# Kernel tuning notes

Measured on AMD Instinct MI355X. Metric: run time of the kernel, lower is better.

The kernel has to match this reference:

```python
import jax, jax.numpy as jnp
import numpy as np

T, N, H, K, A = 256, 8, 512, 16, 4
NUM_ACTIONS = 6
P_SUB = 0.1
LOSS_FACTOR = 0.1


def setup_inputs() -> dict:
    key = jax.random.key(0)
    ks = jax.random.split(key, 14)
    inp = {
        "vision": jax.random.normal(ks[0], (T, N, H), dtype=jnp.float32),
        "belief_features": jax.random.normal(ks[1], (T, N, H), dtype=jnp.float32),
        "actions": jax.random.randint(ks[2], (T, N), 0, NUM_ACTIONS + 1),
        # episode-boundary indices per env, kept in [1, T) to match torch slicing semantics
        "env_zeros": jnp.sort(jax.random.randint(ks[3], (N, 4), 1, T), axis=-1),
        "negative_inds": jax.random.randint(ks[4], (T * N,), 0, T * N),
        # params
        "emb": jax.random.normal(ks[5], (NUM_ACTIONS + 1, A), dtype=jnp.float32) * 0.1,
        "W_ih": jax.random.normal(ks[6], (3 * H, A), dtype=jnp.float32) * 0.1,
        "W_hh": jax.random.normal(ks[7], (3 * H, H), dtype=jnp.float32) * 0.02,
        "b_ih": jnp.zeros((3 * H,), jnp.float32),
        "b_hh": jnp.zeros((3 * H,), jnp.float32),
        "W1": jax.random.normal(ks[8], (32, 2 * H), dtype=jnp.float32) * 0.02,
        "b1": jnp.zeros((32,), jnp.float32),
        "W2": jax.random.normal(ks[9], (1, 32), dtype=jnp.float32) * 0.1,
        "b2": jnp.zeros((1,), jnp.float32),
        "t": T,
        "n": N,
    }
    return inp


def reference(vision, belief_features, actions, env_zeros, negative_inds,
              emb, W_ih, W_hh, b_ih, b_hh, W1, b1, W2, b2, t, n):
    k = K
    h = vision.shape[-1]
    dt = vision.dtype

    positives = vision                                     # (t, n, H)
    negatives = vision.reshape(t * n, h)[negative_inds].reshape(t, n, h)

    # action sequences via unfold: act_seq[m, i*n+e] = padded[i+m, e]
    act_emb = emb[actions]                                 # (t, n, A)
    act_pad = jnp.concatenate([act_emb, jnp.zeros((k - 1, n, A), dt)], axis=0)
    idx = jnp.arange(t)[:, None] + jnp.arange(k)[None, :]  # (t, k)
    act_seq = act_pad[idx].transpose(1, 0, 2, 3).reshape(k, t * n, A)

    # GRU (torch gate order: r, z, n), h0 = belief features per (t,n) position
    h0 = belief_features.reshape(t * n, h)

    def gru_step(hs, x):
        gi = x @ W_ih.T + b_ih
        gh = hs @ W_hh.T + b_hh
        i_r, i_z, i_n = jnp.split(gi, 3, axis=-1)
        h_r, h_z, h_n = jnp.split(gh, 3, axis=-1)
        r = jax.nn.sigmoid(i_r + h_r)
        z = jax.nn.sigmoid(i_z + h_z)
        cand = jnp.tanh(i_n + r * h_n)
        h_new = (1.0 - z) * cand + z * hs
        return h_new, h_new

    _, out_all = jax.lax.scan(gru_step, h0, act_seq)       # (k, t*n, H)
    query_all = out_all.reshape(k, t, n, h).transpose(1, 0, 2, 3)  # (t, k, n, H)

    zpad = jnp.zeros((k, n, h), dt)
    pos_exp = jnp.concatenate([positives[1:], zpad], axis=0)[idx]  # (t, k, n, H)
    neg_exp = jnp.concatenate([negatives[1:], zpad], axis=0)[idx]

    def classify(feat):
        h1 = jax.nn.relu(feat @ W1.T + b1)
        return (h1 @ W2.T + b2)[..., 0]                    # (t, k, n)

    pos_logits = classify(jnp.concatenate([pos_exp, query_all], axis=-1))
    neg_logits = classify(jnp.concatenate([neg_exp, query_all], axis=-1))

    # valid mask: valid_full[r, c, e] then take diagonals valid[i, m, e] = valid_full[i+m, m, e]
    r = jnp.arange(t + k)[:, None, None]                   # (t+k, 1, 1)
    c = jnp.arange(k)[None, :, None]                       # (1, k, 1)
    z = env_zeros[None, None, :, :]                        # (1, 1, n, m)
    zero_hit = jnp.any((z >= (r - c + 1)[..., None]) & (z <= (r + 1)[..., None]), axis=-1)
    valid_full = (r >= c) & (r < t - 1) & (~zero_hit)      # (t+k, k, n)
    valid_mask = valid_full[idx, jnp.arange(k)[None, :]]   # (t, k, n)

    weight = jnp.array([5, 4, 3, 3, 2, 2, 2, 2, 1, 1, 1, 1, 1, 1, 1, 1], dtype=dt)

    # BCE-with-logits: target 1 -> softplus(-x); target 0 -> softplus(x)
    pos_loss = jax.nn.softplus(-pos_logits) * weight[None, :, None]
    neg_loss = jax.nn.softplus(neg_logits) * weight[None, :, None]

    k1, k2 = jax.random.split(jax.random.key(42))
    sub_p = jax.random.uniform(k1, pos_loss.shape) < P_SUB
    sub_n = jax.random.uniform(k2, neg_loss.shape) < P_SUB

    def masked_mean(loss, mask):
        m = mask.astype(dt)
        return jnp.sum(loss * m) / jnp.maximum(jnp.sum(m), 1.0)

    sp = masked_mean(pos_loss, valid_mask & sub_p)
    sn = masked_mean(neg_loss, valid_mask & sub_n)
    return (sp + sn) * LOSS_FACTOR
```

## Files before the change

### kernel.cpp

```cpp
#include <hip/hip_runtime.h>
#include <hip/hip_bf16.h>

#define T_DIM 256
#define KK    16

typedef __attribute__((ext_vector_type(8))) short bf16x8;
typedef __attribute__((ext_vector_type(4))) float f32x4;

#define MFMA16(A, B, C) __builtin_amdgcn_mfma_f32_16x16x32_bf16(A, B, C, 0, 0, 0)
#define SLOT 1048576

__device__ __forceinline__ unsigned short f2b(float x) {
  unsigned u = __float_as_uint(x);
  unsigned r = (u + 0x7FFFu + ((u >> 16) & 1u)) >> 16;
  return (unsigned short)r;
}

__device__ __forceinline__ bf16x8 ld_b128_bypass(const unsigned short* p) {
  bf16x8 r;
  asm volatile("global_load_dwordx4 %0, %1, off sc0 sc1" : "=v"(r) : "v"(p) : "memory");
  return r;
}
__device__ __forceinline__ void st_b128_bypass(unsigned short* p, bf16x8 v) {
  asm volatile("global_store_dwordx4 %0, %1, off sc0 sc1" :: "v"(p), "v"(v) : "memory");
}
__device__ __forceinline__ unsigned ld_u32_bypass(const unsigned* p) {
  unsigned r;
  asm volatile("global_load_dword %0, %1, off sc0 sc1\n\ts_waitcnt vmcnt(0)"
               : "=v"(r) : "v"(p) : "memory");
  return r;
}
__device__ __forceinline__ bf16x8 ld_b128(const unsigned short* p) {
  bf16x8 r;
  asm volatile("global_load_dwordx4 %0, %1, off" : "=v"(r) : "v"(p) : "memory");
  return r;
}
#define WAITVM0() asm volatile("s_waitcnt vmcnt(0)" ::: "memory")

__device__ __forceinline__ void tf2x32(unsigned k0, unsigned k1, unsigned x0, unsigned x1,
                                       unsigned &o0, unsigned &o1) {
  unsigned ks2 = k0 ^ k1 ^ 0x1BD11BDAu;
  x0 += k0; x1 += k1;
#define TFR(R) { x0 += x1; x1 = (x1 << R) | (x1 >> (32 - R)); x1 ^= x0; }
  TFR(13) TFR(15) TFR(26) TFR(6)   x0 += k1;  x1 += ks2 + 1u;
  TFR(17) TFR(29) TFR(16) TFR(24)  x0 += ks2; x1 += k0 + 2u;
  TFR(13) TFR(15) TFR(26) TFR(6)   x0 += k0;  x1 += k1 + 3u;
  TFR(17) TFR(29) TFR(16) TFR(24)  x0 += k1;  x1 += ks2 + 4u;
  TFR(13) TFR(15) TFR(26) TFR(6)   x0 += ks2; x1 += k0 + 5u;
#undef TFR
  o0 = x0; o1 = x1;
}

__global__ void prep(const float* __restrict__ W_hh, const float* __restrict__ W1,
                     const float* __restrict__ emb,  const float* __restrict__ W_ih,
                     const float* __restrict__ b_ih, const float* __restrict__ b_hh,
                     const float* __restrict__ vision, const int* __restrict__ env_zeros,
                     const float* __restrict__ belief,
                     unsigned short* __restrict__ wBf, unsigned short* __restrict__ wQf,
                     float* __restrict__ girz, float* __restrict__ gin,
                     float* __restrict__ projP, unsigned char* __restrict__ maskb,
                     unsigned short* __restrict__ hbS, unsigned* __restrict__ cnt) {
  int b = blockIdx.x, tid = threadIdx.x;
  if (b < 768) {
    int idx = b * 256 + tid;
    int row = idx >> 7, k4 = (idx & 127) << 2;
    float4 v = *(const float4*)(W_hh + ((size_t)row << 9) + k4);
    int gam = row >> 9, sl = (row >> 6) & 7, q = (row >> 4) & 3, col0 = row & 15;
    int kt = k4 >> 5, quad = (k4 >> 3) & 3, e = k4 & 7;
    int F = (sl * 12 + gam * 4 + q) * 16 + kt;
    ushort4 o; o.x = f2b(v.x); o.y = f2b(v.y); o.z = f2b(v.z); o.w = f2b(v.w);
    *(ushort4*)(wBf + ((size_t)F << 9) + ((quad * 16 + col0) << 3) + e) = o;
  } else if (b < 784) {
    int idx = (b - 768) * 256 + tid;
    int f = idx >> 7, k4 = (idx & 127) << 2;
    float4 v = *(const float4*)(W1 + (size_t)f * 1024 + 512 + k4);
    int ft = f >> 4, col0 = f & 15;
    int kt = k4 >> 5, quad = (k4 >> 3) & 3, e = k4 & 7;
    int F = ft * 16 + kt;
    ushort4 o; o.x = f2b(v.x); o.y = f2b(v.y); o.z = f2b(v.z); o.w = f2b(v.w);
    *(ushort4*)(wQf + ((size_t)F << 9) + ((quad * 16 + col0) << 3) + e) = o;
  } else if (b < 816) {
    int idx = (b - 784) * 256 + tid;
    int c = idx & 511, ga = idx >> 9;
    int a = ga & 7, gam = ga >> 3;
    float s = b_ih[gam * 512 + c] + b_hh[gam * 512 + c];
    if (a < 7) {
      #pragma unroll
      for (int k = 0; k < 4; ++k) s += emb[a * 4 + k] * W_ih[(gam * 512 + c) * 4 + k];
    }
    girz[idx] = s;
  } else if (b < 832) {
    int idx = (b - 816) * 256 + tid;
    int c = idx & 511, a = idx >> 9;
    float s = b_ih[1024 + c];
    if (a < 7) {
      #pragma unroll
      for (int k = 0; k < 4; ++k) s += emb[a * 4 + k] * W_ih[(1024 + c) * 4 + k];
    }
    gin[idx] = s;
  } else if (b < 1088) {
    int e = (b - 832) * 256 + tid;
    int s = e >> 5, f = e & 31;
    const float4* vr = (const float4*)(vision + (size_t)s * 512);
    const float4* wr = (const float4*)(W1 + (size_t)f * 1024);
    float a0 = 0.f, a1 = 0.f;
    for (int i = 0; i < 128; i += 2) {
      float4 x = vr[i], w = wr[i];
      float4 y = vr[i + 1], u = wr[i + 1];
      a0 += x.x * w.x + x.y * w.y + x.z * w.z + x.w * w.w;
      a1 += y.x * u.x + y.y * u.y + y.z * u.z + y.w * u.w;
    }
    projP[e] = a0 + a1;
  } else if (b < 1152) {
    int i = (b - 1088) * 256 + tid;
    unsigned a0, b0, a1, b1_;
    tf2x32(0u, 42u, 0u, 2u, a0, b0);
    tf2x32(0u, 42u, 1u, 3u, a1, b1_);
    unsigned p0, p1, n0, n1;
    tf2x32(a0, a1, (unsigned)i, (unsigned)(i + 16384), p0, p1);
    tf2x32(b0, b1_, (unsigned)i, (unsigned)(i + 16384), n0, n1);
    #pragma unroll
    for (int h = 0; h < 2; ++h) {
      int f = i + h * 16384;
      unsigned pw = h ? p1 : p0, nw = h ? n1 : n0;
      int t = f >> 7, j = (f >> 3) & 15, nn = f & 7;
      int ok = (t + j < T_DIM - 1);
      if (ok) {
        int lo = t + 1, hi = t + j + 1, hit = 0;
        #pragma unroll
        for (int q = 0; q < 4; ++q) { int z = env_zeros[nn * 4 + q]; hit |= (z >= lo && z <= hi); }
        ok = !hit;
      }
      unsigned sp = ((pw >> 9) < 0xCCCCDu) ? 1u : 0u;
      unsigned sn = ((nw >> 9) < 0xCCCCDu) ? 2u : 0u;
      maskb[f] = ok ? (unsigned char)(sp | sn) : (unsigned char)0;
    }
  } else if (b == 1152) {
    for (int i = tid; i < 1024; i += 256) cnt[i] = 0u;
  } else {
    int i = (b - 1153) * 256 + tid;
    int f = i >> 6, l = i & 63;
    int seq = (f >> 4) * 16 + (l & 15);
    int kb = (f & 15) * 32 + (l >> 4) * 8;
    const float* src = belief + (size_t)seq * 512 + kb;
    float4 v0 = *(const float4*)src, v1 = *(const float4*)(src + 4);
    bf16x8 o;
    o[0] = (short)f2b(v0.x); o[1] = (short)f2b(v0.y); o[2] = (short)f2b(v0.z); o[3] = (short)f2b(v0.w);
    o[4] = (short)f2b(v1.x); o[5] = (short)f2b(v1.y); o[6] = (short)f2b(v1.z); o[7] = (short)f2b(v1.w);
    *(bf16x8*)&hbS[((size_t)f << 9) + l * 8] = o;
  }
}

__global__ __launch_bounds__(384, 1) void gru_main(
    const float* __restrict__ belief, const int* __restrict__ actions,
    const float* __restrict__ b_hh, const unsigned short* __restrict__ wBf,
    const float* __restrict__ girz, const float* __restrict__ gin,
    unsigned short* __restrict__ hbS, unsigned* __restrict__ cnt) {
  __shared__ char smem[65536];
  __shared__ float hpL[64][68];
  unsigned short* sA = (unsigned short*)smem;
  float* accL = (float*)smem;
  unsigned short* bounce = (unsigned short*)(smem + 49152);

  const int tid = threadIdx.x, w = tid >> 6, lane = tid & 63;
  const int b = blockIdx.x;
  const int sl = b >> 5, g = b & 31;
  const int c0 = sl * 64, seqbase = g * 64;

  bf16x8 bB[32];
  {
    const unsigned short* p0 = wBf + ((size_t)((sl * 12 + 2 * w) * 16) << 9) + lane * 8;
    #pragma unroll
    for (int kt = 0; kt < 32; ++kt) bB[kt] = ld_b128(p0 + ((size_t)kt << 9));
    WAITVM0();
  }

  #pragma unroll
  for (int k = 0; k < 11; ++k) {
    int e = tid + 384 * k;
    if (e < 4096) {
      int s = e >> 6, c = e & 63;
      hpL[s][c] = belief[((size_t)(seqbase + s) << 9) + c0 + c];
    }
  }

  for (int j = 0; j < KK; ++j) {
    if (j > 0) {
      if (tid == 0) {
        const unsigned tgt = 8u * (unsigned)j;
        while (ld_u32_bypass(cnt + g * 32) < tgt) __builtin_amdgcn_s_sleep(1);
      }
      __syncthreads();
    }
    {
      const unsigned short* src = hbS + (size_t)j * SLOT + ((size_t)(g * 64) << 9);
      int line[11];
      bf16x8 tv[11];
      #pragma unroll
      for (int k = 0; k < 11; ++k) line[k] = ((tid + 384 * k) + sl * 512) & 4095;
      #pragma unroll
      for (int k = 0; k < 10; ++k) tv[k] = ld_b128_bypass(src + ((size_t)line[k] << 3));
      const bool ex = (tid < 256);
      if (ex) tv[10] = ld_b128_bypass(src + ((size_t)line[10] << 3));
      WAITVM0();
      #pragma unroll
      for (int k = 0; k < 10; ++k) *(bf16x8*)&sA[(size_t)line[k] << 3] = tv[k];
      if (ex) *(bf16x8*)&sA[(size_t)line[10] << 3] = tv[10];
    }
    __syncthreads();

    f32x4 acc[4][2];
    #pragma unroll
    for (int a = 0; a < 4; ++a) { acc[a][0] = (f32x4){0,0,0,0}; acc[a][1] = (f32x4){0,0,0,0}; }
    #pragma unroll
    for (int kt = 0; kt < 16; ++kt) {
      #pragma unroll
      for (int a = 0; a < 4; ++a) {
        bf16x8 af = *(const bf16x8*)&sA[((a * 16 + kt) << 9) + (lane << 3)];
        acc[a][0] = MFMA16(af, bB[kt], acc[a][0]);
        acc[a][1] = MFMA16(af, bB[16 + kt], acc[a][1]);
      }
    }
    __syncthreads();

    #pragma unroll
    for (int t2 = 0; t2 < 2; ++t2)
      #pragma unroll
      for (int a = 0; a < 4; ++a)
        *(f32x4*)&accL[(((w * 2 + t2) * 4 + a) * 64 + lane) * 4] = acc[a][t2];
    __syncthreads();

    #pragma unroll
    for (int k = 0; k < 11; ++k) {
      int e = tid + 384 * k;
      if (e < 4096) {
        int s = e >> 6, c = e & 63;
        int q = c >> 4, a = s >> 4, m = s & 15;
        int li = (((m >> 2) * 16 + (c & 15)) << 2) + (m & 3);
        float aR = accL[((q * 4 + a) << 8) + li];
        float aZ = accL[(((4 + q) * 4 + a) << 8) + li];
        float aN = accL[(((8 + q) * 4 + a) << 8) + li];
        int seq = seqbase + s;
        int tr = seq >> 3, nn = seq & 7, tj = tr + j;
        int ai = (tj < T_DIM) ? actions[tj * 8 + nn] : 7;
        int cc = c0 + c;
        float rg = 1.f / (1.f + __expf(-(aR + girz[(ai << 9) + cc])));
        float zg = 1.f / (1.f + __expf(-(aZ + girz[((8 + ai) << 9) + cc])));
        float pre = gin[(ai << 9) + cc] + rg * (aN + b_hh[1024 + cc]);
        float cand = 1.f - 2.f / (1.f + __expf(2.f * pre));
        float hn = (1.f - zg) * cand + zg * hpL[s][c];
        hpL[s][c] = hn;
        bounce[s * 72 + c] = f2b(hn);
      }
    }
    __syncthreads();

    unsigned short* dst = hbS + (size_t)(j + 1) * SLOT;
    {
      int f = tid >> 6, l = tid & 63;
      int a = f >> 1, ktl = f & 1;
      bf16x8 v = *(const bf16x8*)&bounce[(16 * a + (l & 15)) * 72 + 32 * ktl + (l >> 4) * 8];
      st_b128_bypass(&dst[((size_t)(g * 64 + a * 16 + sl * 2 + ktl) << 9) + (l << 3)], v);
      if (tid < 128) {
        int i2 = tid + 384;
        int f2 = i2 >> 6, l2 = i2 & 63;
        int a2 = f2 >> 1, ktl2 = f2 & 1;
        bf16x8 v2 = *(const bf16x8*)&bounce[(16 * a2 + (l2 & 15)) * 72 + 32 * ktl2 + (l2 >> 4) * 8];
        st_b128_bypass(&dst[((size_t)(g * 64 + a2 * 16 + sl * 2 + ktl2) << 9) + (l2 << 3)], v2);
      }
    }
    WAITVM0();
    __syncthreads();
    if (tid == 0) atomicAdd(cnt + g * 32, 1u);
  }
}

__global__ __launch_bounds__(256, 1) void cls(
    const unsigned short* __restrict__ hbS, const unsigned short* __restrict__ wQf,
    const int* __restrict__ neg_inds, const float* __restrict__ b1,
    const float* __restrict__ W2, const float* __restrict__ b2,
    const float* __restrict__ projP, const unsigned char* __restrict__ maskb,
    float* __restrict__ parts) {
  __shared__ float red[4][4];
  const int g = blockIdx.x >> 4, jq = blockIdx.x & 15;
  const int w = threadIdx.x >> 6, lane = threadIdx.x & 63;
  const int col0 = lane & 15, quad = lane >> 4;
  const int a = w, j = jq + 1;
  const unsigned short* hsrc = hbS + (size_t)j * SLOT + ((size_t)(g * 64 + a * 16) << 9);
  const unsigned short* qp = wQf + lane * 8;
  f32x4 acc0 = {0,0,0,0}, acc1 = {0,0,0,0};
  #pragma unroll
  for (int kt = 0; kt < 16; ++kt) {
    bf16x8 af = *(const bf16x8*)&hsrc[((size_t)kt << 9) + lane * 8];
    acc0 = MFMA16(af, *(const bf16x8*)(qp + ((size_t)kt << 9)), acc0);
    acc1 = MFMA16(af, *(const bf16x8*)(qp + ((size_t)(16 + kt) << 9)), acc1);
  }
  float b1v0 = b1[col0], b1v1 = b1[col0 + 16];
  float w2v0 = W2[col0], w2v1 = W2[col0 + 16], b2v = b2[0];
  float wj = (jq == 0) ? 5.f : (jq == 1) ? 4.f : (jq < 4) ? 3.f : (jq < 8) ? 2.f : 1.f;
  float sumP = 0.f, cntP = 0.f, sumN = 0.f, cntN = 0.f;
  #pragma unroll
  for (int r = 0; r < 4; ++r) {
    int seq = g * 64 + 16 * a + quad * 4 + r;
    int t = seq >> 3, nn = seq & 7;
    unsigned mb = maskb[(t << 7) + (jq << 3) + nn];
    float pp0 = 0.f, pp1 = 0.f, pn0 = 0.f, pn1 = 0.f;
    if (mb) {
      int sp = seq + j * 8;
      pp0 = projP[(sp << 5) + col0];  pp1 = projP[(sp << 5) + 16 + col0];
      int ni = neg_inds[sp];
      pn0 = projP[(ni << 5) + col0];  pn1 = projP[(ni << 5) + 16 + col0];
    }
    float a0v = acc0[r] + b1v0, a1v = acc1[r] + b1v1;
    float pl = fmaxf(a0v + pp0, 0.f) * w2v0 + fmaxf(a1v + pp1, 0.f) * w2v1;
    float nl = fmaxf(a0v + pn0, 0.f) * w2v0 + fmaxf(a1v + pn1, 0.f) * w2v1;
    #pragma unroll
    for (int d = 1; d < 16; d <<= 1) { pl += __shfl_xor(pl, d, 64); nl += __shfl_xor(nl, d, 64); }
    if (col0 == 0 && mb) {
      if (mb & 1u) {
        float x = -(pl + b2v);
        sumP += wj * (fmaxf(x, 0.f) + __logf(1.f + __expf(-fabsf(x))));
        cntP += 1.f;
      }
      if (mb & 2u) {
        float x = (nl + b2v);
        sumN += wj * (fmaxf(x, 0.f) + __logf(1.f + __expf(-fabsf(x))));
        cntN += 1.f;
      }
    }
  }
  #pragma unroll
  for (int d = 16; d < 64; d <<= 1) {
    sumP += __shfl_xor(sumP, d, 64); cntP += __shfl_xor(cntP, d, 64);
    sumN += __shfl_xor(sumN, d, 64); cntN += __shfl_xor(cntN, d, 64);
  }
  if (lane == 0) { red[w][0] = sumP; red[w][1] = cntP; red[w][2] = sumN; red[w][3] = cntN; }
  __syncthreads();
  if (threadIdx.x < 4)
    parts[blockIdx.x * 4 + threadIdx.x] =
        red[0][threadIdx.x] + red[1][threadIdx.x] + red[2][threadIdx.x] + red[3][threadIdx.x];
}

__global__ __launch_bounds__(256, 1) void fin(const float* __restrict__ parts,
                                              float* __restrict__ out) {
  __shared__ float red[4][4];
  const int tid = threadIdx.x;
  float v0 = 0.f, v1 = 0.f, v2 = 0.f, v3 = 0.f;
  for (int i = tid; i < 512; i += 256) {
    v0 += parts[i * 4 + 0]; v1 += parts[i * 4 + 1];
    v2 += parts[i * 4 + 2]; v3 += parts[i * 4 + 3];
  }
  #pragma unroll
  for (int d = 1; d < 64; d <<= 1) {
    v0 += __shfl_xor(v0, d, 64); v1 += __shfl_xor(v1, d, 64);
    v2 += __shfl_xor(v2, d, 64); v3 += __shfl_xor(v3, d, 64);
  }
  if ((tid & 63) == 0) {
    int w = tid >> 6;
    red[w][0] = v0; red[w][1] = v1; red[w][2] = v2; red[w][3] = v3;
  }
  __syncthreads();
  if (tid == 0) {
    float sP = red[0][0] + red[1][0] + red[2][0] + red[3][0];
    float cP = red[0][1] + red[1][1] + red[2][1] + red[3][1];
    float sN = red[0][2] + red[1][2] + red[2][2] + red[3][2];
    float cN = red[0][3] + red[1][3] + red[2][3] + red[3][3];
    out[0] = (sP / fmaxf(cP, 1.f) + sN / fmaxf(cN, 1.f)) * 0.1f;
  }
}

extern "C" void kernel_launch(void* const* d_in, const int* in_sizes, int n_in,
                              void* d_out, int out_size, void* d_ws, size_t ws_size,
                              hipStream_t stream) {
  const float* vision  = (const float*)d_in[0];
  const float* belief  = (const float*)d_in[1];
  const int*   actions = (const int*)d_in[2];
  const int*   envz    = (const int*)d_in[3];
  const int*   negi    = (const int*)d_in[4];
  const float* emb     = (const float*)d_in[5];
  const float* W_ih    = (const float*)d_in[6];
  const float* W_hh    = (const float*)d_in[7];
  const float* b_ih    = (const float*)d_in[8];
  const float* b_hh    = (const float*)d_in[9];
  const float* W1      = (const float*)d_in[10];
  const float* b1      = (const float*)d_in[11];
  const float* W2      = (const float*)d_in[12];
  const float* b2      = (const float*)d_in[13];

  char* ws = (char*)d_ws;
  unsigned*       cnt   = (unsigned*)(ws + 0);
  float*          parts = (float*)(ws + 4096);
  unsigned short* wBf   = (unsigned short*)(ws + 12288);
  unsigned short* wQf   = (unsigned short*)(ws + 1585152);
  float*          girz  = (float*)(ws + 1617920);
  float*          gin   = (float*)(ws + 1650688);
  float*          projP = (float*)(ws + 1667072);
  unsigned char*  maskb = (unsigned char*)(ws + 1929216);
  unsigned short* hbS   = (unsigned short*)(ws + 1961984);

  prep<<<1665, 256, 0, stream>>>(W_hh, W1, emb, W_ih, b_ih, b_hh, vision, envz,
                                 belief, wBf, wQf, girz, gin, projP, maskb,
                                 hbS, cnt);
  gru_main<<<256, 384, 0, stream>>>(belief, actions, b_hh, wBf, girz, gin,
                                    hbS, cnt);
  cls<<<512, 256, 0, stream>>>(hbS, wQf, negi, b1, W2, b2, projP, maskb, parts);
  fin<<<1, 256, 0, stream>>>(parts, (float*)d_out);
}
```

Measured before the change: 279.5 us.

## Fuse classifier into GRU kernel, split state loads, restructure projection and layouts

Removes the separate classifier kernel. The GRU blocks with sl<4 now compute each step's classifier logits and BCE loss from the hidden-state tile already staged in shared memory, and write the partial sums straight to parts. The per-step global load of the hidden state is split into two halves so the second half's loads overlap the first half's MFMAs. The hbS tile layout and the LDS accumulator layout change (padded, per-wave rows) to match. The vision·W1 projection in prep is redone as one block per sequence with a shared-memory reduction across 8 K-chunks, and the sleep interval in the spin-wait changes. The fused classifier adds serial work to a quarter of the blocks inside the dependency chain and raises LDS usage.

Result: slower. 450.5 us (+61.2%).

```diff
diff --git a/kernel.cpp b/kernel.cpp
--- a/kernel.cpp
+++ b/kernel.cpp
@@ -98,21 +98,8 @@
       for (int k = 0; k < 4; ++k) s += emb[a * 4 + k] * W_ih[(1024 + c) * 4 + k];
     }
     gin[idx] = s;
-  } else if (b < 1088) {
-    int e = (b - 832) * 256 + tid;
-    int s = e >> 5, f = e & 31;
-    const float4* vr = (const float4*)(vision + (size_t)s * 512);
-    const float4* wr = (const float4*)(W1 + (size_t)f * 1024);
-    float a0 = 0.f, a1 = 0.f;
-    for (int i = 0; i < 128; i += 2) {
-      float4 x = vr[i], w = wr[i];
-      float4 y = vr[i + 1], u = wr[i + 1];
-      a0 += x.x * w.x + x.y * w.y + x.z * w.z + x.w * w.w;
-      a1 += y.x * u.x + y.y * u.y + y.z * u.z + y.w * u.w;
-    }
-    projP[e] = a0 + a1;
-  } else if (b < 1152) {
-    int i = (b - 1088) * 256 + tid;
+  } else if (b < 896) {
+    int i = (b - 832) * 256 + tid;
     unsigned a0, b0, a1, b1_;
     tf2x32(0u, 42u, 0u, 2u, a0, b0);
     tf2x32(0u, 42u, 1u, 3u, a1, b1_);
@@ -135,19 +122,40 @@
       unsigned sn = ((nw >> 9) < 0xCCCCDu) ? 2u : 0u;
       maskb[f] = ok ? (unsigned char)(sp | sn) : (unsigned char)0;
     }
-  } else if (b == 1152) {
+  } else if (b == 896) {
     for (int i = tid; i < 1024; i += 256) cnt[i] = 0u;
-  } else {
-    int i = (b - 1153) * 256 + tid;
+  } else if (b < 1409) {
+    int i = (b - 897) * 256 + tid;
     int f = i >> 6, l = i & 63;
-    int seq = (f >> 4) * 16 + (l & 15);
-    int kb = (f & 15) * 32 + (l >> 4) * 8;
+    int f2 = f & 63;
+    int seq = (f >> 6) * 64 + (f2 & 3) * 16 + (l & 15);
+    int kb = (f2 >> 2) * 32 + (l >> 4) * 8;
     const float* src = belief + (size_t)seq * 512 + kb;
     float4 v0 = *(const float4*)src, v1 = *(const float4*)(src + 4);
     bf16x8 o;
     o[0] = (short)f2b(v0.x); o[1] = (short)f2b(v0.y); o[2] = (short)f2b(v0.z); o[3] = (short)f2b(v0.w);
     o[4] = (short)f2b(v1.x); o[5] = (short)f2b(v1.y); o[6] = (short)f2b(v1.z); o[7] = (short)f2b(v1.w);
     *(bf16x8*)&hbS[((size_t)f << 9) + l * 8] = o;
+  } else {
+    __shared__ float red[32][9];
+    int s = b - 1409;
+    int f = tid & 31, kc = tid >> 5;
+    const float4* wr = (const float4*)(W1 + (size_t)f * 1024 + kc * 64);
+    const float4* vr = (const float4*)(vision + (size_t)s * 512 + kc * 64);
+    float acc = 0.f;
+    #pragma unroll
+    for (int i = 0; i < 16; ++i) {
+      float4 wv = wr[i], vv = vr[i];
+      acc += wv.x * vv.x + wv.y * vv.y + wv.z * vv.z + wv.w * vv.w;
+    }
+    red[f][kc] = acc;
+    __syncthreads();
+    if (kc == 0) {
+      float t = 0.f;
+      #pragma unroll
+      for (int q = 0; q < 8; ++q) t += red[f][q];
+      projP[s * 32 + f] = t;
+    }
   }
 }
 
@@ -155,17 +163,21 @@
     const float* __restrict__ belief, const int* __restrict__ actions,
     const float* __restrict__ b_hh, const unsigned short* __restrict__ wBf,
     const float* __restrict__ girz, const float* __restrict__ gin,
-    unsigned short* __restrict__ hbS, unsigned* __restrict__ cnt) {
-  __shared__ char smem[65536];
-  __shared__ float hpL[64][68];
-  unsigned short* sA = (unsigned short*)smem;
-  float* accL = (float*)smem;
-  unsigned short* bounce = (unsigned short*)(smem + 49152);
+    unsigned short* __restrict__ hbS, unsigned* __restrict__ cnt,
+    const unsigned short* __restrict__ wQf, const int* __restrict__ neg_inds,
+    const float* __restrict__ b1, const float* __restrict__ W2,
+    const float* __restrict__ b2, const float* __restrict__ projP,
+    const unsigned char* __restrict__ maskb, float* __restrict__ parts) {
+  __shared__ unsigned short sA[64 * 512];
+  __shared__ float accL2[12672];
+  __shared__ unsigned short bounce[64 * 74];
+  __shared__ float hpL[64 * 66];
 
   const int tid = threadIdx.x, w = tid >> 6, lane = tid & 63;
   const int b = blockIdx.x;
   const int sl = b >> 5, g = b & 31;
   const int c0 = sl * 64, seqbase = g * 64;
+  const int col0 = lane & 15, quad = lane >> 4;
 
   bf16x8 bB[32];
   {
@@ -177,168 +189,187 @@
 
   #pragma unroll
   for (int k = 0; k < 11; ++k) {
-    int e = tid + 384 * k;
-    if (e < 4096) {
-      int s = e >> 6, c = e & 63;
-      hpL[s][c] = belief[((size_t)(seqbase + s) << 9) + c0 + c];
-    }
-  }
-
-  for (int j = 0; j < KK; ++j) {
+    int s = 6 * k + w;
+    if (s < 64) hpL[s * 66 + lane] = belief[((size_t)(seqbase + s) << 9) + c0 + lane];
+  }
+
+  const float b1v0 = b1[col0], b1v1 = b1[col0 + 16];
+  const float w2v0 = W2[col0], w2v1 = W2[col0 + 16], b2v = b2[0];
+  float sumP = 0.f, cntP = 0.f, sumN = 0.f, cntN = 0.f;
+
+  for (int j = 0; j <= KK; ++j) {
     if (j > 0) {
       if (tid == 0) {
         const unsigned tgt = 8u * (unsigned)j;
-        while (ld_u32_bypass(cnt + g * 32) < tgt) __builtin_amdgcn_s_sleep(1);
+        while (ld_u32_bypass(cnt + g * 32) < tgt) __builtin_amdgcn_s_sleep(2);
       }
       __syncthreads();
     }
+    const unsigned short* src = hbS + (size_t)j * SLOT + ((size_t)(g * 64) << 9);
     {
-      const unsigned short* src = hbS + (size_t)j * SLOT + ((size_t)(g * 64) << 9);
-      int line[11];
-      bf16x8 tv[11];
-      #pragma unroll
-      for (int k = 0; k < 11; ++k) line[k] = ((tid + 384 * k) + sl * 512) & 4095;
-      #pragma unroll
-      for (int k = 0; k < 10; ++k) tv[k] = ld_b128_bypass(src + ((size_t)line[k] << 3));
-      const bool ex = (tid < 256);
-      if (ex) tv[10] = ld_b128_bypass(src + ((size_t)line[10] << 3));
+      bf16x8 u0 = ld_b128_bypass(src + ((size_t)(tid)        << 3));
+      bf16x8 u1 = ld_b128_bypass(src + ((size_t)(tid + 384)  << 3));
+      bf16x8 u2 = ld_b128_bypass(src + ((size_t)(tid + 768)  << 3));
+      bf16x8 u3 = ld_b128_bypass(src + ((size_t)(tid + 1152) << 3));
+      bf16x8 u4 = ld_b128_bypass(src + ((size_t)(tid + 1536) << 3));
+      bf16x8 u5; const bool ex = (tid < 128);
+      if (ex) u5 = ld_b128_bypass(src + ((size_t)(tid + 1920) << 3));
       WAITVM0();
-      #pragma unroll
-      for (int k = 0; k < 10; ++k) *(bf16x8*)&sA[(size_t)line[k] << 3] = tv[k];
-      if (ex) *(bf16x8*)&sA[(size_t)line[10] << 3] = tv[10];
-    }
+      *(bf16x8*)&sA[(size_t)(tid)        << 3] = u0;
+      *(bf16x8*)&sA[(size_t)(tid + 384)  << 3] = u1;
+      *(bf16x8*)&sA[(size_t)(tid + 768)  << 3] = u2;
+      *(bf16x8*)&sA[(size_t)(tid + 1152) << 3] = u3;
+      *(bf16x8*)&sA[(size_t)(tid + 1536) << 3] = u4;
+      if (ex) *(bf16x8*)&sA[(size_t)(tid + 1920) << 3] = u5;
+    }
+    bf16x8 v0 = ld_b128_bypass(src + ((size_t)(tid + 2048) << 3));
+    bf16x8 v1 = ld_b128_bypass(src + ((size_t)(tid + 2432) << 3));
+    bf16x8 v2 = ld_b128_bypass(src + ((size_t)(tid + 2816) << 3));
+    bf16x8 v3 = ld_b128_bypass(src + ((size_t)(tid + 3200) << 3));
+    bf16x8 v4 = ld_b128_bypass(src + ((size_t)(tid + 3584) << 3));
+    bf16x8 v5; const bool ex2 = (tid < 128);
+    if (ex2) v5 = ld_b128_bypass(src + ((size_t)(tid + 3968) << 3));
     __syncthreads();
 
     f32x4 acc[4][2];
     #pragma unroll
     for (int a = 0; a < 4; ++a) { acc[a][0] = (f32x4){0,0,0,0}; acc[a][1] = (f32x4){0,0,0,0}; }
+    if (j < KK) {
+      #pragma unroll
+      for (int kt = 0; kt < 8; ++kt) {
+        #pragma unroll
+        for (int a = 0; a < 4; ++a) {
+          bf16x8 af = *(const bf16x8*)&sA[(((kt * 4 + a)) << 9) + (lane << 3)];
+          acc[a][0] = MFMA16(af, bB[kt], acc[a][0]);
+          acc[a][1] = MFMA16(af, bB[16 + kt], acc[a][1]);
+        }
+      }
+    }
+    WAITVM0();
+    *(bf16x8*)&sA[(size_t)(tid + 2048) << 3] = v0;
+    *(bf16x8*)&sA[(size_t)(tid + 2432) << 3] = v1;
+    *(bf16x8*)&sA[(size_t)(tid + 2816) << 3] = v2;
+    *(bf16x8*)&sA[(size_t)(tid + 3200) << 3] = v3;
+    *(bf16x8*)&sA[(size_t)(tid + 3584) << 3] = v4;
+    if (ex2) *(bf16x8*)&sA[(size_t)(tid + 3968) << 3] = v5;
+    __syncthreads();
+
+    if (j < KK) {
+      #pragma unroll
+      for (int kt = 8; kt < 16; ++kt) {
+        #pragma unroll
+        for (int a = 0; a < 4; ++a) {
+          bf16x8 af = *(const bf16x8*)&sA[(((kt * 4 + a)) << 9) + (lane << 3)];
+          acc[a][0] = MFMA16(af, bB[kt], acc[a][0]);
+          acc[a][1] = MFMA16(af, bB[16 + kt], acc[a][1]);
+        }
+      }
+      #pragma unroll
+      for (int t2 = 0; t2 < 2; ++t2) {
+        int nu = w * 2 + t2, gam = nu >> 2, q = nu & 3;
+        #pragma unroll
+        for (int a = 0; a < 4; ++a)
+          #pragma unroll
+          for (int r = 0; r < 4; ++r)
+            accL2[((gam * 4 + a) * 16 + quad * 4 + r) * 66 + q * 16 + col0] = acc[a][t2][r];
+      }
+      __syncthreads();
+      #pragma unroll
+      for (int k = 0; k < 11; ++k) {
+        int s = 6 * k + w;
+        if (s < 64) {
+          int c = lane, a = s >> 4, m = s & 15;
+          int cc = c0 + c;
+          float aR = accL2[((a) * 16 + m) * 66 + c];
+          float aZ = accL2[((4 + a) * 16 + m) * 66 + c];
+          float aN = accL2[((8 + a) * 16 + m) * 66 + c];
+          int seq = seqbase + s;
+          int tr = seq >> 3, nn = seq & 7, tj = tr + j;
+          int ai = (tj < T_DIM) ? actions[tj * 8 + nn] : 7;
+          float rg = 1.f / (1.f + __expf(-(aR + girz[(ai << 9) + cc])));
+          float zg = 1.f / (1.f + __expf(-(aZ + girz[((8 + ai) << 9) + cc])));
+          float pre = gin[(ai << 9) + cc] + rg * (aN + b_hh[1024 + cc]);
+          float cand = 1.f - 2.f / (1.f + __expf(2.f * pre));
+          float hn = (1.f - zg) * cand + zg * hpL[s * 66 + c];
+          hpL[s * 66 + c] = hn;
+          bounce[s * 74 + c] = f2b(hn);
+        }
+      }
+      __syncthreads();
+      unsigned short* dst = hbS + (size_t)(j + 1) * SLOT;
+      {
+        int f = tid >> 6, l = tid & 63;
+        int a = f >> 1, ktl = f & 1;
+        bf16x8 vv = *(const bf16x8*)&bounce[(16 * a + (l & 15)) * 74 + 32 * ktl + (l >> 4) * 8];
+        st_b128_bypass(&dst[((size_t)(g * 64 + (2 * sl + ktl) * 4 + a) << 9) + (l << 3)], vv);
+        if (tid < 128) {
+          int i2 = tid + 384;
+          int f2 = i2 >> 6, l2 = i2 & 63;
+          int a2 = f2 >> 1, ktl2 = f2 & 1;
+          bf16x8 v2b = *(const bf16x8*)&bounce[(16 * a2 + (l2 & 15)) * 74 + 32 * ktl2 + (l2 >> 4) * 8];
+          st_b128_bypass(&dst[((size_t)(g * 64 + (2 * sl + ktl2) * 4 + a2) << 9) + (l2 << 3)], v2b);
+        }
+      }
+      WAITVM0();
+      __syncthreads();
+      if (tid == 0) atomicAdd(cnt + g * 32, 1u);
+    }
+
+    if (j >= 1 && sl < 4 && w == 0) {
+      const int jq = j - 1, a = sl;
+      const unsigned short* qp = wQf + lane * 8;
+      f32x4 ca0 = {0,0,0,0}, ca1 = {0,0,0,0};
+      #pragma unroll
+      for (int kt = 0; kt < 16; ++kt) {
+        bf16x8 af = *(const bf16x8*)&sA[((kt * 4 + a) << 9) + (lane << 3)];
+        ca0 = MFMA16(af, *(const bf16x8*)(qp + ((size_t)kt << 9)), ca0);
+        ca1 = MFMA16(af, *(const bf16x8*)(qp + ((size_t)(16 + kt) << 9)), ca1);
+      }
+      float wj = (jq == 0) ? 5.f : (jq == 1) ? 4.f : (jq < 4) ? 3.f : (jq < 8) ? 2.f : 1.f;
+      #pragma unroll
+      for (int r = 0; r < 4; ++r) {
+        int seq = seqbase + 16 * a + quad * 4 + r;
+        int t = seq >> 3, nn = seq & 7;
+        unsigned mb = maskb[(t << 7) + (jq << 3) + nn];
+        float pp0 = 0.f, pp1 = 0.f, pn0 = 0.f, pn1 = 0.f;
+        if (mb) {
+          int sp = seq + j * 8;
+          pp0 = projP[(sp << 5) + col0];  pp1 = projP[(sp << 5) + 16 + col0];
+          int ni = neg_inds[sp];
+          pn0 = projP[(ni << 5) + col0];  pn1 = projP[(ni << 5) + 16 + col0];
+        }
+        float a0v = ca0[r] + b1v0, a1v = ca1[r] + b1v1;
+        float pl = fmaxf(a0v + pp0, 0.f) * w2v0 + fmaxf(a1v + pp1, 0.f) * w2v1;
+        float nl = fmaxf(a0v + pn0, 0.f) * w2v0 + fmaxf(a1v + pn1, 0.f) * w2v1;
+        #pragma unroll
+        for (int d = 1; d < 16; d <<= 1) { pl += __shfl_xor(pl, d, 64); nl += __shfl_xor(nl, d, 64); }
+        if (col0 == 0 && mb) {
+          if (mb & 1u) {
+            float x = -(pl + b2v);
+            sumP += wj * (fmaxf(x, 0.f) + __logf(1.f + __expf(-fabsf(x))));
+            cntP += 1.f;
+          }
+          if (mb & 2u) {
+            float x = (nl + b2v);
+            sumN += wj * (fmaxf(x, 0.f) + __logf(1.f + __expf(-fabsf(x))));
+            cntN += 1.f;
+          }
+        }
+      }
+    }
+  }
+
+  if (sl < 4 && w == 0) {
     #pragma unroll
-    for (int kt = 0; kt < 16; ++kt) {
-      #pragma unroll
-      for (int a = 0; a < 4; ++a) {
-        bf16x8 af = *(const bf16x8*)&sA[((a * 16 + kt) << 9) + (lane << 3)];
-        acc[a][0] = MFMA16(af, bB[kt], acc[a][0]);
-        acc[a][1] = MFMA16(af, bB[16 + kt], acc[a][1]);
-      }
-    }
-    __syncthreads();
-
-    #pragma unroll
-    for (int t2 = 0; t2 < 2; ++t2)
-      #pragma unroll
-      for (int a = 0; a < 4; ++a)
-        *(f32x4*)&accL[(((w * 2 + t2) * 4 + a) * 64 + lane) * 4] = acc[a][t2];
-    __syncthreads();
-
-    #pragma unroll
-    for (int k = 0; k < 11; ++k) {
-      int e = tid + 384 * k;
-      if (e < 4096) {
-        int s = e >> 6, c = e & 63;
-        int q = c >> 4, a = s >> 4, m = s & 15;
-        int li = (((m >> 2) * 16 + (c & 15)) << 2) + (m & 3);
-        float aR = accL[((q * 4 + a) << 8) + li];
-        float aZ = accL[(((4 + q) * 4 + a) << 8) + li];
-        float aN = accL[(((8 + q) * 4 + a) << 8) + li];
-        int seq = seqbase + s;
-        int tr = seq >> 3, nn = seq & 7, tj = tr + j;
-        int ai = (tj < T_DIM) ? actions[tj * 8 + nn] : 7;
-        int cc = c0 + c;
-        float rg = 1.f / (1.f + __expf(-(aR + girz[(ai << 9) + cc])));
-        float zg = 1.f / (1.f + __expf(-(aZ + girz[((8 + ai) << 9) + cc])));
-        float pre = gin[(ai << 9) + cc] + rg * (aN + b_hh[1024 + cc]);
-        float cand = 1.f - 2.f / (1.f + __expf(2.f * pre));
-        float hn = (1.f - zg) * cand + zg * hpL[s][c];
-        hpL[s][c] = hn;
-        bounce[s * 72 + c] = f2b(hn);
-      }
-    }
-    __syncthreads();
-
-    unsigned short* dst = hbS + (size_t)(j + 1) * SLOT;
-    {
-      int f = tid >> 6, l = tid & 63;
-      int a = f >> 1, ktl = f & 1;
-      bf16x8 v = *(const bf16x8*)&bounce[(16 * a + (l & 15)) * 72 + 32 * ktl + (l >> 4) * 8];
-      st_b128_bypass(&dst[((size_t)(g * 64 + a * 16 + sl * 2 + ktl) << 9) + (l << 3)], v);
-      if (tid < 128) {
-        int i2 = tid + 384;
-        int f2 = i2 >> 6, l2 = i2 & 63;
-        int a2 = f2 >> 1, ktl2 = f2 & 1;
-        bf16x8 v2 = *(const bf16x8*)&bounce[(16 * a2 + (l2 & 15)) * 72 + 32 * ktl2 + (l2 >> 4) * 8];
-        st_b128_bypass(&dst[((size_t)(g * 64 + a2 * 16 + sl * 2 + ktl2) << 9) + (l2 << 3)], v2);
-      }
-    }
-    WAITVM0();
-    __syncthreads();
-    if (tid == 0) atomicAdd(cnt + g * 32, 1u);
-  }
-}
-
-__global__ __launch_bounds__(256, 1) void cls(
-    const unsigned short* __restrict__ hbS, const unsigned short* __restrict__ wQf,
-    const int* __restrict__ neg_inds, const float* __restrict__ b1,
-    const float* __restrict__ W2, const float* __restrict__ b2,
-    const float* __restrict__ projP, const unsigned char* __restrict__ maskb,
-    float* __restrict__ parts) {
-  __shared__ float red[4][4];
-  const int g = blockIdx.x >> 4, jq = blockIdx.x & 15;
-  const int w = threadIdx.x >> 6, lane = threadIdx.x & 63;
-  const int col0 = lane & 15, quad = lane >> 4;
-  const int a = w, j = jq + 1;
-  const unsigned short* hsrc = hbS + (size_t)j * SLOT + ((size_t)(g * 64 + a * 16) << 9);
-  const unsigned short* qp = wQf + lane * 8;
-  f32x4 acc0 = {0,0,0,0}, acc1 = {0,0,0,0};
-  #pragma unroll
-  for (int kt = 0; kt < 16; ++kt) {
-    bf16x8 af = *(const bf16x8*)&hsrc[((size_t)kt << 9) + lane * 8];
-    acc0 = MFMA16(af, *(const bf16x8*)(qp + ((size_t)kt << 9)), acc0);
-    acc1 = MFMA16(af, *(const bf16x8*)(qp + ((size_t)(16 + kt) << 9)), acc1);
-  }
-  float b1v0 = b1[col0], b1v1 = b1[col0 + 16];
-  float w2v0 = W2[col0], w2v1 = W2[col0 + 16], b2v = b2[0];
-  float wj = (jq == 0) ? 5.f : (jq == 1) ? 4.f : (jq < 4) ? 3.f : (jq < 8) ? 2.f : 1.f;
-  float sumP = 0.f, cntP = 0.f, sumN = 0.f, cntN = 0.f;
-  #pragma unroll
-  for (int r = 0; r < 4; ++r) {
-    int seq = g * 64 + 16 * a + quad * 4 + r;
-    int t = seq >> 3, nn = seq & 7;
-    unsigned mb = maskb[(t << 7) + (jq << 3) + nn];
-    float pp0 = 0.f, pp1 = 0.f, pn0 = 0.f, pn1 = 0.f;
-    if (mb) {
-      int sp = seq + j * 8;
-      pp0 = projP[(sp << 5) + col0];  pp1 = projP[(sp << 5) + 16 + col0];
-      int ni = neg_inds[sp];
-      pn0 = projP[(ni << 5) + col0];  pn1 = projP[(ni << 5) + 16 + col0];
-    }
-    float a0v = acc0[r] + b1v0, a1v = acc1[r] + b1v1;
-    float pl = fmaxf(a0v + pp0, 0.f) * w2v0 + fmaxf(a1v + pp1, 0.f) * w2v1;
-    float nl = fmaxf(a0v + pn0, 0.f) * w2v0 + fmaxf(a1v + pn1, 0.f) * w2v1;
-    #pragma unroll
-    for (int d = 1; d < 16; d <<= 1) { pl += __shfl_xor(pl, d, 64); nl += __shfl_xor(nl, d, 64); }
-    if (col0 == 0 && mb) {
-      if (mb & 1u) {
-        float x = -(pl + b2v);
-        sumP += wj * (fmaxf(x, 0.f) + __logf(1.f + __expf(-fabsf(x))));
-        cntP += 1.f;
-      }
-      if (mb & 2u) {
-        float x = (nl + b2v);
-        sumN += wj * (fmaxf(x, 0.f) + __logf(1.f + __expf(-fabsf(x))));
-        cntN += 1.f;
-      }
-    }
-  }
-  #pragma unroll
-  for (int d = 16; d < 64; d <<= 1) {
-    sumP += __shfl_xor(sumP, d, 64); cntP += __shfl_xor(cntP, d, 64);
-    sumN += __shfl_xor(sumN, d, 64); cntN += __shfl_xor(cntN, d, 64);
-  }
-  if (lane == 0) { red[w][0] = sumP; red[w][1] = cntP; red[w][2] = sumN; red[w][3] = cntN; }
-  __syncthreads();
-  if (threadIdx.x < 4)
-    parts[blockIdx.x * 4 + threadIdx.x] =
-        red[0][threadIdx.x] + red[1][threadIdx.x] + red[2][threadIdx.x] + red[3][threadIdx.x];
+    for (int d = 16; d < 64; d <<= 1) {
+      sumP += __shfl_xor(sumP, d, 64); cntP += __shfl_xor(cntP, d, 64);
+      sumN += __shfl_xor(sumN, d, 64); cntN += __shfl_xor(cntN, d, 64);
+    }
+    if (lane == 0) {
+      float4 o; o.x = sumP; o.y = cntP; o.z = sumN; o.w = cntN;
+      *(float4*)&parts[(sl * 32 + g) * 4] = o;
+    }
+  }
 }
 
 __global__ __launch_bounds__(256, 1) void fin(const float* __restrict__ parts,
@@ -346,9 +377,9 @@
   __shared__ float red[4][4];
   const int tid = threadIdx.x;
   float v0 = 0.f, v1 = 0.f, v2 = 0.f, v3 = 0.f;
-  for (int i = tid; i < 512; i += 256) {
-    v0 += parts[i * 4 + 0]; v1 += parts[i * 4 + 1];
-    v2 += parts[i * 4 + 2]; v3 += parts[i * 4 + 3];
+  if (tid < 128) {
+    v0 = parts[tid * 4 + 0]; v1 = parts[tid * 4 + 1];
+    v2 = parts[tid * 4 + 2]; v3 = parts[tid * 4 + 3];
   }
   #pragma unroll
   for (int d = 1; d < 64; d <<= 1) {
@@ -398,11 +429,11 @@
   unsigned char*  maskb = (unsigned char*)(ws + 1929216);
   unsigned short* hbS   = (unsigned short*)(ws + 1961984);
 
-  prep<<<1665, 256, 0, stream>>>(W_hh, W1, emb, W_ih, b_ih, b_hh, vision, envz,
+  prep<<<3457, 256, 0, stream>>>(W_hh, W1, emb, W_ih, b_ih, b_hh, vision, envz,
                                  belief, wBf, wQf, girz, gin, projP, maskb,
                                  hbS, cnt);
   gru_main<<<256, 384, 0, stream>>>(belief, actions, b_hh, wBf, girz, gin,
-                                    hbS, cnt);
-  cls<<<512, 256, 0, stream>>>(hbS, wQf, negi, b1, W2, b2, projP, maskb, parts);
+                                    hbS, cnt, wQf, negi, b1, W2, b2, projP,
+                                    maskb, parts);
   fin<<<1, 256, 0, stream>>>(parts, (float*)d_out);
 }
```
